# Optimization experiments

Measured on AMD Instinct MI355X. Metric: run time of the kernel, lower is better.

Reference implementation:

```python
import jax, jax.numpy as jnp
import numpy as np

TEMPERATURE = 8.0  # d_k ** 0.5 with d_k = 64
NEG_INF = -1.0e9


def setup_inputs() -> dict:
    key = jax.random.key(0)
    kq, kk, kv, km = jax.random.split(key, 4)
    B, H, L, D = 2, 16, 2048, 64
    q = jax.random.normal(kq, (B, H, L, D), dtype=jnp.float32)
    k = jax.random.normal(kk, (B, H, L, D), dtype=jnp.float32)
    v = jax.random.normal(kv, (B, H, L, D), dtype=jnp.float32)
    mask = jax.random.randint(km, (B, 1, L, L), 0, 2, dtype=jnp.int32)
    return {"q": q, "k": k, "v": v, "mask": mask}


def reference(q, k, v, mask):
    # scores: [B, H, Lq, Lk]
    scores = jnp.einsum("bhqd,bhkd->bhqk", q / TEMPERATURE, k)
    scores = jnp.where(mask == 0, NEG_INF, scores)
    attn = jax.nn.softmax(scores, axis=-1)  # dropout is identity in eval mode
    out = jnp.einsum("bhqk,bhkd->bhqd", attn, v)
    return (out, attn)
```

## Files before the change

### kernel.cpp

```cpp
#include <hip/hip_runtime.h>

#define L_ 2048
#define D_ 64

typedef __attribute__((ext_vector_type(8))) short bf16x8;
typedef __attribute__((ext_vector_type(4))) float f32x4;
typedef __attribute__((ext_vector_type(8))) _Float16 f16x8;
typedef __attribute__((ext_vector_type(2))) _Float16 f16x2;

__device__ __forceinline__ unsigned short f2bf(float x) {
  union { float f; unsigned u; } v; v.f = x;
  return (unsigned short)((v.u + 0x7fffu + ((v.u >> 16) & 1u)) >> 16);
}
__device__ __forceinline__ float bf2f(unsigned short h) {
  union { unsigned u; float f; } v; v.u = ((unsigned)h) << 16; return v.f;
}

__global__ __launch_bounds__(256) void ksplit(const float* __restrict__ k,
                                              unsigned short* __restrict__ kh,
                                              unsigned short* __restrict__ kl) {
  size_t o = ((size_t)blockIdx.x * 256 + threadIdx.x) * 8;
  #pragma unroll
  for (int j = 0; j < 8; ++j) {
    float x = k[o + j];
    unsigned short h = f2bf(x);
    kh[o + j] = h;
    kl[o + j] = f2bf(x - bf2f(h));
  }
}

__global__ __launch_bounds__(256) void vtrans(const float* __restrict__ v,
                                              _Float16* __restrict__ vt) {
  __shared__ _Float16 T[64][72];
  const int blk = blockIdx.x;
  const int bh  = blk >> 5;
  const int k0  = (blk & 31) << 6;
  const int tid = threadIdx.x;
  const float* vb = v + (size_t)bh * (L_ * D_) + (size_t)k0 * D_;
  const int r = tid >> 4, c4 = (tid & 15) << 2;
  #pragma unroll
  for (int p = 0; p < 4; ++p) {
    float4 u = *(const float4*)(vb + (size_t)(r + p * 16) * D_ + c4);
    T[r + p * 16][c4 + 0] = (_Float16)u.x;
    T[r + p * 16][c4 + 1] = (_Float16)u.y;
    T[r + p * 16][c4 + 2] = (_Float16)u.z;
    T[r + p * 16][c4 + 3] = (_Float16)u.w;
  }
  __syncthreads();
  _Float16* vo = vt + (size_t)bh * (D_ * L_);
  const int d = tid >> 2, kk = (tid & 3) << 4;
  f16x8 w0, w1;
  #pragma unroll
  for (int j = 0; j < 8; ++j) { w0[j] = T[kk + j][d]; w1[j] = T[kk + 8 + j][d]; }
  *(f16x8*)(vo + (size_t)d * L_ + k0 + kk) = w0;
  *(f16x8*)(vo + (size_t)d * L_ + k0 + kk + 8) = w1;
}

__device__ __forceinline__ void split4(const float4 u, float sc, bf16x8& h, bf16x8& l, int o) {
  float s; unsigned short hh;
  s = u.x * sc; hh = f2bf(s); h[o+0] = (short)hh; l[o+0] = (short)f2bf(s - bf2f(hh));
  s = u.y * sc; hh = f2bf(s); h[o+1] = (short)hh; l[o+1] = (short)f2bf(s - bf2f(hh));
  s = u.z * sc; hh = f2bf(s); h[o+2] = (short)hh; l[o+2] = (short)f2bf(s - bf2f(hh));
  s = u.w * sc; hh = f2bf(s); h[o+3] = (short)hh; l[o+3] = (short)f2bf(s - bf2f(hh));
}

template<bool USE_WS, bool USE_VT>
__global__ __launch_bounds__(256, 4) void attn_fused(
    const float* __restrict__ qf, const float* __restrict__ kf,
    const unsigned short* __restrict__ khp, const unsigned short* __restrict__ klp,
    const int* __restrict__ mask, const float* __restrict__ vf,
    const _Float16* __restrict__ vtp_g,
    float* __restrict__ outp, float* __restrict__ attnp) {
  __shared__ __align__(16) unsigned int Wst[4][16 * 20];
  __shared__ float Ored[4][16][64];
  __shared__ float red[16][5];
  __shared__ float rowL[16];

  const int tid  = threadIdx.x;
  const int p    = blockIdx.x;
  const int wg   = ((p & 7) << 9) | (p >> 3);
  const int bh   = wg >> 7;
  const int q0   = (wg & 127) << 4;
  const int b    = bh >> 4;
  const int lane = tid & 63;
  const int wave = tid >> 6;
  const int c16  = lane & 15;
  const int quad = lane >> 4;

  bf16x8 a0h, a0l, a1h, a1l;
  {
    const float* qp = qf + ((size_t)(bh * L_ + q0 + c16)) * D_ + (quad << 3);
    split4(*(const float4*)qp,        0.125f, a0h, a0l, 0);
    split4(*(const float4*)(qp + 4),  0.125f, a0h, a0l, 4);
    split4(*(const float4*)(qp + 32), 0.125f, a1h, a1l, 0);
    split4(*(const float4*)(qp + 36), 0.125f, a1h, a1l, 4);
  }

  const int qrow = q0 + c16;
  const int* mbase = mask + ((size_t)(b * L_) + qrow) * L_ + (wave << 9) + (quad << 2);

  const unsigned short* hpb = nullptr;
  const unsigned short* lpb = nullptr;
  const float* kfb = nullptr;
  if (USE_WS) {
    hpb = khp + (size_t)bh * (L_ * D_) + ((size_t)((wave << 9) + c16)) * D_ + (quad << 3);
    lpb = klp + (size_t)bh * (L_ * D_) + ((size_t)((wave << 9) + c16)) * D_ + (quad << 3);
  } else {
    kfb = kf + (size_t)bh * (L_ * D_) + ((size_t)((wave << 9) + c16)) * D_ + (quad << 3);
  }

  f16x2 E[64];
  float lsum = 0.f;

  #pragma unroll
  for (int ct = 0; ct < 32; ++ct) {
    bf16x8 b0h, b1h, b0l, b1l;
    if (USE_WS) {
      const unsigned short* hp = hpb + ct * (16 * D_);
      const unsigned short* lp = lpb + ct * (16 * D_);
      b0h = *(const bf16x8*)(hp);
      b1h = *(const bf16x8*)(hp + 32);
      b0l = *(const bf16x8*)(lp);
      b1l = *(const bf16x8*)(lp + 32);
    } else {
      const float* kp = kfb + ct * (16 * D_);
      #pragma unroll
      for (int j = 0; j < 4; ++j) {
        float x0 = kp[j], x1 = kp[4 + j], x2 = kp[32 + j], x3 = kp[36 + j];
        b0h[j]     = (short)f2bf(x0); b0l[j]     = (short)f2bf(x0 - bf2f((unsigned short)b0h[j]));
        b0h[4 + j] = (short)f2bf(x1); b0l[4 + j] = (short)f2bf(x1 - bf2f((unsigned short)b0h[4 + j]));
        b1h[j]     = (short)f2bf(x2); b1l[j]     = (short)f2bf(x2 - bf2f((unsigned short)b1h[j]));
        b1h[4 + j] = (short)f2bf(x3); b1l[4 + j] = (short)f2bf(x3 - bf2f((unsigned short)b1h[4 + j]));
      }
    }
    const int4 mk = *(const int4*)(mbase + (ct << 4));
    f32x4 acc1 = {-6.f, -6.f, -6.f, -6.f};
    f32x4 acc2 = {0.f, 0.f, 0.f, 0.f};
    __builtin_amdgcn_s_setprio(1);
    acc1 = __builtin_amdgcn_mfma_f32_16x16x32_bf16(b0h, a0h, acc1, 0, 0, 0);
    acc2 = __builtin_amdgcn_mfma_f32_16x16x32_bf16(b1h, a1h, acc2, 0, 0, 0);
    acc1 = __builtin_amdgcn_mfma_f32_16x16x32_bf16(b0l, a0h, acc1, 0, 0, 0);
    acc2 = __builtin_amdgcn_mfma_f32_16x16x32_bf16(b1l, a1h, acc2, 0, 0, 0);
    acc1 = __builtin_amdgcn_mfma_f32_16x16x32_bf16(b0h, a0l, acc1, 0, 0, 0);
    acc2 = __builtin_amdgcn_mfma_f32_16x16x32_bf16(b1h, a1l, acc2, 0, 0, 0);
    __builtin_amdgcn_s_setprio(0);
    float e0 = mk.x ? __expf(acc1[0] + acc2[0]) : 0.f;
    float e1 = mk.y ? __expf(acc1[1] + acc2[1]) : 0.f;
    float e2 = mk.z ? __expf(acc1[2] + acc2[2]) : 0.f;
    float e3 = mk.w ? __expf(acc1[3] + acc2[3]) : 0.f;
    lsum += (e0 + e1) + (e2 + e3);
    E[2 * ct]     = f16x2{(_Float16)e0, (_Float16)e1};
    E[2 * ct + 1] = f16x2{(_Float16)e2, (_Float16)e3};
  }

  lsum += __shfl_xor(lsum, 16);
  lsum += __shfl_xor(lsum, 32);
  if (lane < 16) red[lane][wave] = lsum;
  __syncthreads();
  if (tid < 16) {
    float l = red[tid][0] + red[tid][1] + red[tid][2] + red[tid][3];
    rowL[tid] = (l > 0.f) ? (1.f / l) : 0.f;
  }
  __syncthreads();
  const float inv = rowL[c16];

  float* abase = attnp + ((size_t)(bh * L_) + qrow) * L_ + (wave << 9) + (quad << 2);
  unsigned int* Wp = &Wst[wave][0];
  const int wr = c16 * 20;
  const _Float16* vt0 = nullptr;
  if (USE_VT) vt0 = vtp_g + (size_t)bh * (D_ * L_) + (size_t)c16 * L_ + (wave << 9) + (quad << 3);
  f32x4 o0 = {0.f, 0.f, 0.f, 0.f}, o1 = o0, o2 = o0, o3 = o0;

  #pragma unroll
  for (int c = 0; c < 16; ++c) {
    Wp[wr + (quad << 1) + 0]     = __builtin_bit_cast(unsigned int, E[4 * c + 0]);
    Wp[wr + (quad << 1) + 1]     = __builtin_bit_cast(unsigned int, E[4 * c + 1]);
    Wp[wr + 8 + (quad << 1) + 0] = __builtin_bit_cast(unsigned int, E[4 * c + 2]);
    Wp[wr + 8 + (quad << 1) + 1] = __builtin_bit_cast(unsigned int, E[4 * c + 3]);
    f32x4 pa = { (float)E[4 * c + 0][0] * inv, (float)E[4 * c + 0][1] * inv,
                 (float)E[4 * c + 1][0] * inv, (float)E[4 * c + 1][1] * inv };
    f32x4 pb = { (float)E[4 * c + 2][0] * inv, (float)E[4 * c + 2][1] * inv,
                 (float)E[4 * c + 3][0] * inv, (float)E[4 * c + 3][1] * inv };
    __builtin_nontemporal_store(pa, (f32x4*)(abase + (c << 5)));
    __builtin_nontemporal_store(pb, (f32x4*)(abase + (c << 5) + 16));
    __builtin_amdgcn_wave_barrier();
    const f16x8 A = *(const f16x8*)&Wst[wave][wr + (quad << 2)];
    __builtin_amdgcn_s_setprio(1);
    if (USE_VT) {
      o0 = __builtin_amdgcn_mfma_f32_16x16x32_f16(A, *(const f16x8*)(vt0 + (c << 5)), o0, 0, 0, 0);
      o1 = __builtin_amdgcn_mfma_f32_16x16x32_f16(A, *(const f16x8*)(vt0 + 16 * L_ + (c << 5)), o1, 0, 0, 0);
      o2 = __builtin_amdgcn_mfma_f32_16x16x32_f16(A, *(const f16x8*)(vt0 + 32 * L_ + (c << 5)), o2, 0, 0, 0);
      o3 = __builtin_amdgcn_mfma_f32_16x16x32_f16(A, *(const f16x8*)(vt0 + 48 * L_ + (c << 5)), o3, 0, 0, 0);
    } else {
      const float* vb = vf + (size_t)bh * (L_ * D_);
      const int kb = (wave << 9) + (c << 5) + (quad << 3);
      f16x8 bv0, bv1, bv2, bv3;
      #pragma unroll
      for (int j = 0; j < 8; ++j) {
        const float* vr = vb + (size_t)(kb + j) * D_ + c16;
        bv0[j] = (_Float16)vr[0];
        bv1[j] = (_Float16)vr[16];
        bv2[j] = (_Float16)vr[32];
        bv3[j] = (_Float16)vr[48];
      }
      o0 = __builtin_amdgcn_mfma_f32_16x16x32_f16(A, bv0, o0, 0, 0, 0);
      o1 = __builtin_amdgcn_mfma_f32_16x16x32_f16(A, bv1, o1, 0, 0, 0);
      o2 = __builtin_amdgcn_mfma_f32_16x16x32_f16(A, bv2, o2, 0, 0, 0);
      o3 = __builtin_amdgcn_mfma_f32_16x16x32_f16(A, bv3, o3, 0, 0, 0);
    }
    __builtin_amdgcn_s_setprio(0);
  }

  {
    const int r0 = quad << 2;
    #pragma unroll
    for (int g = 0; g < 4; ++g) {
      Ored[wave][r0 + g][c16]      = o0[g];
      Ored[wave][r0 + g][16 + c16] = o1[g];
      Ored[wave][r0 + g][32 + c16] = o2[g];
      Ored[wave][r0 + g][48 + c16] = o3[g];
    }
  }
  __syncthreads();
  {
    const int r = tid >> 4, d0 = (tid & 15) << 2;
    const float sc = rowL[r];
    f32x4 s = {0.f, 0.f, 0.f, 0.f};
    #pragma unroll
    for (int w = 0; w < 4; ++w) {
      s[0] += Ored[w][r][d0 + 0];
      s[1] += Ored[w][r][d0 + 1];
      s[2] += Ored[w][r][d0 + 2];
      s[3] += Ored[w][r][d0 + 3];
    }
    s[0] *= sc; s[1] *= sc; s[2] *= sc; s[3] *= sc;
    float* dst = outp + ((size_t)(bh * L_ + q0 + r)) * D_ + d0;
    __builtin_nontemporal_store(s, (f32x4*)dst);
  }
}

extern "C" void kernel_launch(void* const* d_in, const int* in_sizes, int n_in,
                              void* d_out, int out_size, void* d_ws, size_t ws_size,
                              hipStream_t stream) {
  const float* q = (const float*)d_in[0];
  const float* k = (const float*)d_in[1];
  const float* v = (const float*)d_in[2];
  const int* mask = (const int*)d_in[3];
  float* outp  = (float*)d_out;
  float* attnp = outp + (size_t)4194304;

  if (ws_size >= (size_t)25165824) {
    unsigned short* kh = (unsigned short*)d_ws;
    unsigned short* kl = kh + (size_t)4194304;
    _Float16* vt = (_Float16*)(kl + (size_t)4194304);
    ksplit<<<2048, 256, 0, stream>>>(k, kh, kl);
    vtrans<<<1024, 256, 0, stream>>>(v, vt);
    attn_fused<true, true><<<4096, 256, 0, stream>>>(q, k, kh, kl, mask, v, vt, outp, attnp);
  } else if (ws_size >= (size_t)16777216) {
    unsigned short* kh = (unsigned short*)d_ws;
    unsigned short* kl = kh + (size_t)4194304;
    ksplit<<<2048, 256, 0, stream>>>(k, kh, kl);
    attn_fused<true, false><<<4096, 256, 0, stream>>>(q, k, kh, kl, mask, v, nullptr, outp, attnp);
  } else {
    attn_fused<false, false><<<4096, 256, 0, stream>>>(q, k, nullptr, nullptr, mask, v, nullptr, outp, attnp);
  }
}
```

Before: 952.1 us.

## Recompute QK^T scores in second pass instead of holding exp values in registers

Drops the 64-element register array of exponentiated scores and recomputes the QK^T MFMAs, mask loads and exps in the PV loop, reducing register pressure. Loop unrolling is also reduced to shrink code and register use. The cost is reloading K fragments and the mask and doubling the score MFMA and exp work. The attn values written now use full-precision exp rather than the fp16-rounded ones.

```diff
diff --git a/kernel.cpp b/kernel.cpp
--- a/kernel.cpp
+++ b/kernel.cpp
@@ -64,6 +64,30 @@
   s = u.w * sc; hh = f2bf(s); h[o+3] = (short)hh; l[o+3] = (short)f2bf(s - bf2f(hh));
 }
 
+template<bool USE_WS>
+__device__ __forceinline__ void load_kfrag(const unsigned short* hpb, const unsigned short* lpb,
+                                           const float* kfb, int ct,
+                                           bf16x8& b0h, bf16x8& b1h, bf16x8& b0l, bf16x8& b1l) {
+  if (USE_WS) {
+    const unsigned short* hp = hpb + ct * (16 * D_);
+    const unsigned short* lp = lpb + ct * (16 * D_);
+    b0h = *(const bf16x8*)(hp);
+    b1h = *(const bf16x8*)(hp + 32);
+    b0l = *(const bf16x8*)(lp);
+    b1l = *(const bf16x8*)(lp + 32);
+  } else {
+    const float* kp = kfb + ct * (16 * D_);
+    #pragma unroll
+    for (int j = 0; j < 4; ++j) {
+      float x0 = kp[j], x1 = kp[4 + j], x2 = kp[32 + j], x3 = kp[36 + j];
+      b0h[j]     = (short)f2bf(x0); b0l[j]     = (short)f2bf(x0 - bf2f((unsigned short)b0h[j]));
+      b0h[4 + j] = (short)f2bf(x1); b0l[4 + j] = (short)f2bf(x1 - bf2f((unsigned short)b0h[4 + j]));
+      b1h[j]     = (short)f2bf(x2); b1l[j]     = (short)f2bf(x2 - bf2f((unsigned short)b1h[j]));
+      b1h[4 + j] = (short)f2bf(x3); b1l[4 + j] = (short)f2bf(x3 - bf2f((unsigned short)b1h[4 + j]));
+    }
+  }
+}
+
 template<bool USE_WS, bool USE_VT>
 __global__ __launch_bounds__(256, 4) void attn_fused(
     const float* __restrict__ qf, const float* __restrict__ kf,
@@ -109,30 +133,11 @@
     kfb = kf + (size_t)bh * (L_ * D_) + ((size_t)((wave << 9) + c16)) * D_ + (quad << 3);
   }
 
-  f16x2 E[64];
   float lsum = 0.f;
-
-  #pragma unroll
+  #pragma unroll 4
   for (int ct = 0; ct < 32; ++ct) {
     bf16x8 b0h, b1h, b0l, b1l;
-    if (USE_WS) {
-      const unsigned short* hp = hpb + ct * (16 * D_);
-      const unsigned short* lp = lpb + ct * (16 * D_);
-      b0h = *(const bf16x8*)(hp);
-      b1h = *(const bf16x8*)(hp + 32);
-      b0l = *(const bf16x8*)(lp);
-      b1l = *(const bf16x8*)(lp + 32);
-    } else {
-      const float* kp = kfb + ct * (16 * D_);
-      #pragma unroll
-      for (int j = 0; j < 4; ++j) {
-        float x0 = kp[j], x1 = kp[4 + j], x2 = kp[32 + j], x3 = kp[36 + j];
-        b0h[j]     = (short)f2bf(x0); b0l[j]     = (short)f2bf(x0 - bf2f((unsigned short)b0h[j]));
-        b0h[4 + j] = (short)f2bf(x1); b0l[4 + j] = (short)f2bf(x1 - bf2f((unsigned short)b0h[4 + j]));
-        b1h[j]     = (short)f2bf(x2); b1l[j]     = (short)f2bf(x2 - bf2f((unsigned short)b1h[j]));
-        b1h[4 + j] = (short)f2bf(x3); b1l[4 + j] = (short)f2bf(x3 - bf2f((unsigned short)b1h[4 + j]));
-      }
-    }
+    load_kfrag<USE_WS>(hpb, lpb, kfb, ct, b0h, b1h, b0l, b1l);
     const int4 mk = *(const int4*)(mbase + (ct << 4));
     f32x4 acc1 = {-6.f, -6.f, -6.f, -6.f};
     f32x4 acc2 = {0.f, 0.f, 0.f, 0.f};
@@ -149,8 +154,6 @@
     float e2 = mk.z ? __expf(acc1[2] + acc2[2]) : 0.f;
     float e3 = mk.w ? __expf(acc1[3] + acc2[3]) : 0.f;
     lsum += (e0 + e1) + (e2 + e3);
-    E[2 * ct]     = f16x2{(_Float16)e0, (_Float16)e1};
-    E[2 * ct + 1] = f16x2{(_Float16)e2, (_Float16)e3};
   }
 
   lsum += __shfl_xor(lsum, 16);
@@ -171,18 +174,35 @@
   if (USE_VT) vt0 = vtp_g + (size_t)bh * (D_ * L_) + (size_t)c16 * L_ + (wave << 9) + (quad << 3);
   f32x4 o0 = {0.f, 0.f, 0.f, 0.f}, o1 = o0, o2 = o0, o3 = o0;
 
-  #pragma unroll
+  #pragma unroll 2
   for (int c = 0; c < 16; ++c) {
-    Wp[wr + (quad << 1) + 0]     = __builtin_bit_cast(unsigned int, E[4 * c + 0]);
-    Wp[wr + (quad << 1) + 1]     = __builtin_bit_cast(unsigned int, E[4 * c + 1]);
-    Wp[wr + 8 + (quad << 1) + 0] = __builtin_bit_cast(unsigned int, E[4 * c + 2]);
-    Wp[wr + 8 + (quad << 1) + 1] = __builtin_bit_cast(unsigned int, E[4 * c + 3]);
-    f32x4 pa = { (float)E[4 * c + 0][0] * inv, (float)E[4 * c + 0][1] * inv,
-                 (float)E[4 * c + 1][0] * inv, (float)E[4 * c + 1][1] * inv };
-    f32x4 pb = { (float)E[4 * c + 2][0] * inv, (float)E[4 * c + 2][1] * inv,
-                 (float)E[4 * c + 3][0] * inv, (float)E[4 * c + 3][1] * inv };
-    __builtin_nontemporal_store(pa, (f32x4*)(abase + (c << 5)));
-    __builtin_nontemporal_store(pb, (f32x4*)(abase + (c << 5) + 16));
+    #pragma unroll
+    for (int h = 0; h < 2; ++h) {
+      const int ct = 2 * c + h;
+      bf16x8 b0h, b1h, b0l, b1l;
+      load_kfrag<USE_WS>(hpb, lpb, kfb, ct, b0h, b1h, b0l, b1l);
+      const int4 mk = *(const int4*)(mbase + (ct << 4));
+      f32x4 acc1 = {-6.f, -6.f, -6.f, -6.f};
+      f32x4 acc2 = {0.f, 0.f, 0.f, 0.f};
+      __builtin_amdgcn_s_setprio(1);
+      acc1 = __builtin_amdgcn_mfma_f32_16x16x32_bf16(b0h, a0h, acc1, 0, 0, 0);
+      acc2 = __builtin_amdgcn_mfma_f32_16x16x32_bf16(b1h, a1h, acc2, 0, 0, 0);
+      acc1 = __builtin_amdgcn_mfma_f32_16x16x32_bf16(b0l, a0h, acc1, 0, 0, 0);
+      acc2 = __builtin_amdgcn_mfma_f32_16x16x32_bf16(b1l, a1h, acc2, 0, 0, 0);
+      acc1 = __builtin_amdgcn_mfma_f32_16x16x32_bf16(b0h, a0l, acc1, 0, 0, 0);
+      acc2 = __builtin_amdgcn_mfma_f32_16x16x32_bf16(b1h, a1l, acc2, 0, 0, 0);
+      __builtin_amdgcn_s_setprio(0);
+      float e0 = mk.x ? __expf(acc1[0] + acc2[0]) : 0.f;
+      float e1 = mk.y ? __expf(acc1[1] + acc2[1]) : 0.f;
+      float e2 = mk.z ? __expf(acc1[2] + acc2[2]) : 0.f;
+      float e3 = mk.w ? __expf(acc1[3] + acc2[3]) : 0.f;
+      Wp[wr + (h << 3) + (quad << 1) + 0] =
+          __builtin_bit_cast(unsigned int, f16x2{(_Float16)e0, (_Float16)e1});
+      Wp[wr + (h << 3) + (quad << 1) + 1] =
+          __builtin_bit_cast(unsigned int, f16x2{(_Float16)e2, (_Float16)e3});
+      f32x4 pa = {e0 * inv, e1 * inv, e2 * inv, e3 * inv};
+      __builtin_nontemporal_store(pa, (f32x4*)(abase + (c << 5) + (h << 4)));
+    }
     __builtin_amdgcn_wave_barrier();
     const f16x8 A = *(const f16x8*)&Wst[wave][wr + (quad << 2)];
     __builtin_amdgcn_s_setprio(1);
```

After: 1.190 ms. 25.0% more time.

## Split each query tile's key range across eight waves instead of four

Applied to the files above, without the earlier changes.

The workgroup grows from 256 to 512 threads, so each wave covers 256 keys instead of 512. This halves the per-wave unrolled loop and the register-held E array (64 to 32 f16x2). The aim is to cut register pressure and add latency hiding per block. In exchange, shared memory for the partial-output reduction doubles, the cross-wave sum runs over eight partials, and the final output store narrows to two floats per thread.

```diff
diff --git a/kernel.cpp b/kernel.cpp
--- a/kernel.cpp
+++ b/kernel.cpp
@@ -5,6 +5,7 @@
 
 typedef __attribute__((ext_vector_type(8))) short bf16x8;
 typedef __attribute__((ext_vector_type(4))) float f32x4;
+typedef __attribute__((ext_vector_type(2))) float f32x2;
 typedef __attribute__((ext_vector_type(8))) _Float16 f16x8;
 typedef __attribute__((ext_vector_type(2))) _Float16 f16x2;
 
@@ -64,16 +65,40 @@
   s = u.w * sc; hh = f2bf(s); h[o+3] = (short)hh; l[o+3] = (short)f2bf(s - bf2f(hh));
 }
 
+template<bool USE_WS>
+__device__ __forceinline__ void load_kfrag(const unsigned short* hpb, const unsigned short* lpb,
+                                           const float* kfb, int ct,
+                                           bf16x8& b0h, bf16x8& b1h, bf16x8& b0l, bf16x8& b1l) {
+  if (USE_WS) {
+    const unsigned short* hp = hpb + ct * (16 * D_);
+    const unsigned short* lp = lpb + ct * (16 * D_);
+    b0h = *(const bf16x8*)(hp);
+    b1h = *(const bf16x8*)(hp + 32);
+    b0l = *(const bf16x8*)(lp);
+    b1l = *(const bf16x8*)(lp + 32);
+  } else {
+    const float* kp = kfb + ct * (16 * D_);
+    #pragma unroll
+    for (int j = 0; j < 4; ++j) {
+      float x0 = kp[j], x1 = kp[4 + j], x2 = kp[32 + j], x3 = kp[36 + j];
+      b0h[j]     = (short)f2bf(x0); b0l[j]     = (short)f2bf(x0 - bf2f((unsigned short)b0h[j]));
+      b0h[4 + j] = (short)f2bf(x1); b0l[4 + j] = (short)f2bf(x1 - bf2f((unsigned short)b0h[4 + j]));
+      b1h[j]     = (short)f2bf(x2); b1l[j]     = (short)f2bf(x2 - bf2f((unsigned short)b1h[j]));
+      b1h[4 + j] = (short)f2bf(x3); b1l[4 + j] = (short)f2bf(x3 - bf2f((unsigned short)b1h[4 + j]));
+    }
+  }
+}
+
 template<bool USE_WS, bool USE_VT>
-__global__ __launch_bounds__(256, 4) void attn_fused(
+__global__ __launch_bounds__(512, 4) void attn_fused(
     const float* __restrict__ qf, const float* __restrict__ kf,
     const unsigned short* __restrict__ khp, const unsigned short* __restrict__ klp,
     const int* __restrict__ mask, const float* __restrict__ vf,
     const _Float16* __restrict__ vtp_g,
     float* __restrict__ outp, float* __restrict__ attnp) {
-  __shared__ __align__(16) unsigned int Wst[4][16 * 20];
-  __shared__ float Ored[4][16][64];
-  __shared__ float red[16][5];
+  __shared__ __align__(16) unsigned int Wst[8][16 * 20];
+  __shared__ float Ored[8][16][66];
+  __shared__ float red[16][9];
   __shared__ float rowL[16];
 
   const int tid  = threadIdx.x;
@@ -97,42 +122,25 @@
   }
 
   const int qrow = q0 + c16;
-  const int* mbase = mask + ((size_t)(b * L_) + qrow) * L_ + (wave << 9) + (quad << 2);
+  const int* mbase = mask + ((size_t)(b * L_) + qrow) * L_ + (wave << 8) + (quad << 2);
 
   const unsigned short* hpb = nullptr;
   const unsigned short* lpb = nullptr;
   const float* kfb = nullptr;
   if (USE_WS) {
-    hpb = khp + (size_t)bh * (L_ * D_) + ((size_t)((wave << 9) + c16)) * D_ + (quad << 3);
-    lpb = klp + (size_t)bh * (L_ * D_) + ((size_t)((wave << 9) + c16)) * D_ + (quad << 3);
+    hpb = khp + (size_t)bh * (L_ * D_) + ((size_t)((wave << 8) + c16)) * D_ + (quad << 3);
+    lpb = klp + (size_t)bh * (L_ * D_) + ((size_t)((wave << 8) + c16)) * D_ + (quad << 3);
   } else {
-    kfb = kf + (size_t)bh * (L_ * D_) + ((size_t)((wave << 9) + c16)) * D_ + (quad << 3);
-  }
-
-  f16x2 E[64];
+    kfb = kf + (size_t)bh * (L_ * D_) + ((size_t)((wave << 8) + c16)) * D_ + (quad << 3);
+  }
+
+  f16x2 E[32];
   float lsum = 0.f;
 
   #pragma unroll
-  for (int ct = 0; ct < 32; ++ct) {
+  for (int ct = 0; ct < 16; ++ct) {
     bf16x8 b0h, b1h, b0l, b1l;
-    if (USE_WS) {
-      const unsigned short* hp = hpb + ct * (16 * D_);
-      const unsigned short* lp = lpb + ct * (16 * D_);
-      b0h = *(const bf16x8*)(hp);
-      b1h = *(const bf16x8*)(hp + 32);
-      b0l = *(const bf16x8*)(lp);
-      b1l = *(const bf16x8*)(lp + 32);
-    } else {
-      const float* kp = kfb + ct * (16 * D_);
-      #pragma unroll
-      for (int j = 0; j < 4; ++j) {
-        float x0 = kp[j], x1 = kp[4 + j], x2 = kp[32 + j], x3 = kp[36 + j];
-        b0h[j]     = (short)f2bf(x0); b0l[j]     = (short)f2bf(x0 - bf2f((unsigned short)b0h[j]));
-        b0h[4 + j] = (short)f2bf(x1); b0l[4 + j] = (short)f2bf(x1 - bf2f((unsigned short)b0h[4 + j]));
-        b1h[j]     = (short)f2bf(x2); b1l[j]     = (short)f2bf(x2 - bf2f((unsigned short)b1h[j]));
-        b1h[4 + j] = (short)f2bf(x3); b1l[4 + j] = (short)f2bf(x3 - bf2f((unsigned short)b1h[4 + j]));
-      }
-    }
+    load_kfrag<USE_WS>(hpb, lpb, kfb, ct, b0h, b1h, b0l, b1l);
     const int4 mk = *(const int4*)(mbase + (ct << 4));
     f32x4 acc1 = {-6.f, -6.f, -6.f, -6.f};
     f32x4 acc2 = {0.f, 0.f, 0.f, 0.f};
@@ -158,31 +166,32 @@
   if (lane < 16) red[lane][wave] = lsum;
   __syncthreads();
   if (tid < 16) {
-    float l = red[tid][0] + red[tid][1] + red[tid][2] + red[tid][3];
+    float l = 0.f;
+    #pragma unroll
+    for (int w = 0; w < 8; ++w) l += red[tid][w];
     rowL[tid] = (l > 0.f) ? (1.f / l) : 0.f;
   }
   __syncthreads();
   const float inv = rowL[c16];
 
-  float* abase = attnp + ((size_t)(bh * L_) + qrow) * L_ + (wave << 9) + (quad << 2);
+  float* abase = attnp + ((size_t)(bh * L_) + qrow) * L_ + (wave << 8) + (quad << 2);
   unsigned int* Wp = &Wst[wave][0];
   const int wr = c16 * 20;
   const _Float16* vt0 = nullptr;
-  if (USE_VT) vt0 = vtp_g + (size_t)bh * (D_ * L_) + (size_t)c16 * L_ + (wave << 9) + (quad << 3);
+  if (USE_VT) vt0 = vtp_g + (size_t)bh * (D_ * L_) + (size_t)c16 * L_ + (wave << 8) + (quad << 3);
   f32x4 o0 = {0.f, 0.f, 0.f, 0.f}, o1 = o0, o2 = o0, o3 = o0;
 
   #pragma unroll
-  for (int c = 0; c < 16; ++c) {
-    Wp[wr + (quad << 1) + 0]     = __builtin_bit_cast(unsigned int, E[4 * c + 0]);
-    Wp[wr + (quad << 1) + 1]     = __builtin_bit_cast(unsigned int, E[4 * c + 1]);
-    Wp[wr + 8 + (quad << 1) + 0] = __builtin_bit_cast(unsigned int, E[4 * c + 2]);
-    Wp[wr + 8 + (quad << 1) + 1] = __builtin_bit_cast(unsigned int, E[4 * c + 3]);
-    f32x4 pa = { (float)E[4 * c + 0][0] * inv, (float)E[4 * c + 0][1] * inv,
-                 (float)E[4 * c + 1][0] * inv, (float)E[4 * c + 1][1] * inv };
-    f32x4 pb = { (float)E[4 * c + 2][0] * inv, (float)E[4 * c + 2][1] * inv,
-                 (float)E[4 * c + 3][0] * inv, (float)E[4 * c + 3][1] * inv };
-    __builtin_nontemporal_store(pa, (f32x4*)(abase + (c << 5)));
-    __builtin_nontemporal_store(pb, (f32x4*)(abase + (c << 5) + 16));
+  for (int c = 0; c < 8; ++c) {
+    #pragma unroll
+    for (int h = 0; h < 2; ++h) {
+      const int ei = (c << 2) + (h << 1);
+      Wp[wr + (h << 3) + (quad << 1) + 0] = __builtin_bit_cast(unsigned int, E[ei]);
+      Wp[wr + (h << 3) + (quad << 1) + 1] = __builtin_bit_cast(unsigned int, E[ei + 1]);
+      f32x4 pa = { (float)E[ei][0] * inv, (float)E[ei][1] * inv,
+                   (float)E[ei + 1][0] * inv, (float)E[ei + 1][1] * inv };
+      __builtin_nontemporal_store(pa, (f32x4*)(abase + (c << 5) + (h << 4)));
+    }
     __builtin_amdgcn_wave_barrier();
     const f16x8 A = *(const f16x8*)&Wst[wave][wr + (quad << 2)];
     __builtin_amdgcn_s_setprio(1);
@@ -193,7 +202,7 @@
       o3 = __builtin_amdgcn_mfma_f32_16x16x32_f16(A, *(const f16x8*)(vt0 + 48 * L_ + (c << 5)), o3, 0, 0, 0);
     } else {
       const float* vb = vf + (size_t)bh * (L_ * D_);
-      const int kb = (wave << 9) + (c << 5) + (quad << 3);
+      const int kb = (wave << 8) + (c << 5) + (quad << 3);
       f16x8 bv0, bv1, bv2, bv3;
       #pragma unroll
       for (int j = 0; j < 8; ++j) {
@@ -223,19 +232,17 @@
   }
   __syncthreads();
   {
-    const int r = tid >> 4, d0 = (tid & 15) << 2;
+    const int r = tid >> 5, d0 = (tid & 31) << 1;
     const float sc = rowL[r];
-    f32x4 s = {0.f, 0.f, 0.f, 0.f};
-    #pragma unroll
-    for (int w = 0; w < 4; ++w) {
+    f32x2 s = {0.f, 0.f};
+    #pragma unroll
+    for (int w = 0; w < 8; ++w) {
       s[0] += Ored[w][r][d0 + 0];
       s[1] += Ored[w][r][d0 + 1];
-      s[2] += Ored[w][r][d0 + 2];
-      s[3] += Ored[w][r][d0 + 3];
-    }
-    s[0] *= sc; s[1] *= sc; s[2] *= sc; s[3] *= sc;
+    }
+    s[0] *= sc; s[1] *= sc;
     float* dst = outp + ((size_t)(bh * L_ + q0 + r)) * D_ + d0;
-    __builtin_nontemporal_store(s, (f32x4*)dst);
+    __builtin_nontemporal_store(s, (f32x2*)dst);
   }
 }
 
@@ -255,13 +262,13 @@
     _Float16* vt = (_Float16*)(kl + (size_t)4194304);
     ksplit<<<2048, 256, 0, stream>>>(k, kh, kl);
     vtrans<<<1024, 256, 0, stream>>>(v, vt);
-    attn_fused<true, true><<<4096, 256, 0, stream>>>(q, k, kh, kl, mask, v, vt, outp, attnp);
+    attn_fused<true, true><<<4096, 512, 0, stream>>>(q, k, kh, kl, mask, v, vt, outp, attnp);
   } else if (ws_size >= (size_t)16777216) {
     unsigned short* kh = (unsigned short*)d_ws;
     unsigned short* kl = kh + (size_t)4194304;
     ksplit<<<2048, 256, 0, stream>>>(k, kh, kl);
-    attn_fused<true, false><<<4096, 256, 0, stream>>>(q, k, kh, kl, mask, v, nullptr, outp, attnp);
+    attn_fused<true, false><<<4096, 512, 0, stream>>>(q, k, kh, kl, mask, v, nullptr, outp, attnp);
   } else {
-    attn_fused<false, false><<<4096, 256, 0, stream>>>(q, k, nullptr, nullptr, mask, v, nullptr, outp, attnp);
-  }
-}
+    attn_fused<false, false><<<4096, 512, 0, stream>>>(q, k, nullptr, nullptr, mask, v, nullptr, outp, attnp);
+  }
+}
```

Result: no change. 941.2 us (-1.1%).
